# Kernel optimization log

Hardware: AMD Instinct MI355X
Metric: run time of the kernel (lower is better)

## Reference

```python
import jax, jax.numpy as jnp
import numpy as np

N_HEAD = 16
ROPE_BASE = 10000.0


def apply_rope(x):
    # x: [B, T, H, D], torchtune interleaved-pair RoPE
    B, T, H, D = x.shape
    pos = jnp.arange(T, dtype=jnp.float32)
    freqs = 1.0 / (ROPE_BASE ** (jnp.arange(0, D, 2, dtype=jnp.float32) / D))  # [D/2]
    theta = pos[:, None] * freqs[None, :]            # [T, D/2]
    cos = jnp.cos(theta)[None, :, None, :]           # [1, T, 1, D/2]
    sin = jnp.sin(theta)[None, :, None, :]
    xp = x.reshape(B, T, H, D // 2, 2)
    x0, x1 = xp[..., 0], xp[..., 1]
    out = jnp.stack([x0 * cos - x1 * sin, x1 * cos + x0 * sin], axis=-1)
    return out.reshape(B, T, H, D).astype(x.dtype)


def setup_inputs() -> dict:
    key = jax.random.key(0)
    k1, k2, k3 = jax.random.split(key, 3)
    B, T, C = 4, 2048, 1024
    x = jax.random.normal(k1, (B, T, C), dtype=jnp.float32)
    w_qkv = jax.random.normal(k2, (C, 3 * C), dtype=jnp.float32) * 0.02
    b_qkv = jnp.zeros((3 * C,), dtype=jnp.float32)
    w_proj = jax.random.normal(k3, (C, C), dtype=jnp.float32) * 0.02
    b_proj = jnp.zeros((C,), dtype=jnp.float32)
    return {"x": x, "w_qkv": w_qkv, "b_qkv": b_qkv, "w_proj": w_proj, "b_proj": b_proj}


def reference(x, w_qkv, b_qkv, w_proj, b_proj):
    B, T, C = x.shape
    H = N_HEAD
    D = C // H
    qkv = x @ w_qkv + b_qkv                          # [B, T, 3C]
    q, k, v = jnp.split(qkv, 3, axis=-1)
    q = apply_rope(q.reshape(B, T, H, D))
    k = apply_rope(k.reshape(B, T, H, D))
    v = v.reshape(B, T, H, D)
    scale = 1.0 / jnp.sqrt(jnp.asarray(D, dtype=x.dtype))
    attn = jnp.einsum('bthd,bshd->bhts', q, k) * scale  # [B, H, T, T] (non-causal)
    attn = jax.nn.softmax(attn, axis=-1)
    out = jnp.einsum('bhts,bshd->bthd', attn, v).reshape(B, T, C)
    return out @ w_proj + b_proj
```

## Files before the change

kernel.cpp:

```cpp
#include <hip/hip_runtime.h>

typedef unsigned short ushort_t;
typedef unsigned int   uint_t;
typedef __attribute__((ext_vector_type(8))) short bf16x8;
typedef __attribute__((ext_vector_type(4))) float f32x4;

__device__ __forceinline__ ushort_t f2bf(float f) {
    union { float f; uint_t i; } x; x.f = f;
    uint_t i = x.i + 0x7fffu + ((x.i >> 16) & 1u);
    return (ushort_t)(i >> 16);
}
__device__ __forceinline__ ushort_t f2bf_trunc(float f) {
    union { float f; uint_t i; } x; x.f = f;
    return (ushort_t)(x.i >> 16);
}
__device__ __forceinline__ void async16(const void* g, void* l) {
    __builtin_amdgcn_global_load_lds(
        (const __attribute__((address_space(1))) uint_t*)g,
        (__attribute__((address_space(3))) uint_t*)l, 16, 0, 0);
}

__global__ __launch_bounds__(256) void conv_bf16(
    const float* __restrict__ in, ushort_t* __restrict__ outp)
{
    int i = (blockIdx.x * 256 + threadIdx.x) * 4;
    float4 v = *(const float4*)(in + i);
    uint_t a = (uint_t)f2bf(v.x) | ((uint_t)f2bf(v.y) << 16);
    uint_t b = (uint_t)f2bf(v.z) | ((uint_t)f2bf(v.w) << 16);
    uint2 st = { a, b };
    *(uint2*)(outp + i) = st;
}

__global__ __launch_bounds__(256) void transpose_conv(
    const float* __restrict__ in, ushort_t* __restrict__ outp, int R, int C)
{
    __shared__ ushort_t t[64][65];
    int r0 = blockIdx.y * 64, c0 = blockIdx.x * 64;
    int lr = threadIdx.x >> 4, lc = (threadIdx.x & 15) * 4;
#pragma unroll
    for (int rr = 0; rr < 4; ++rr) {
        float4 v = *(const float4*)(in + (size_t)(r0 + rr * 16 + lr) * C + c0 + lc);
        t[lc + 0][rr * 16 + lr] = f2bf(v.x);
        t[lc + 1][rr * 16 + lr] = f2bf(v.y);
        t[lc + 2][rr * 16 + lr] = f2bf(v.z);
        t[lc + 3][rr * 16 + lr] = f2bf(v.w);
    }
    __syncthreads();
    int oc = threadIdx.x >> 2, och = (threadIdx.x & 3) * 16;
    union { uint4 v[2]; ushort_t u[16]; } pk;
#pragma unroll
    for (int j = 0; j < 16; ++j) pk.u[j] = t[oc][och + j];
    uint4* dst = (uint4*)(outp + (size_t)(c0 + oc) * R + r0 + och);
    dst[0] = pk.v[0]; dst[1] = pk.v[1];
}

__global__ __launch_bounds__(256) void rope_table_k(float2* __restrict__ tab)
{
    int idx = blockIdx.x * 256 + threadIdx.x;
    int t = idx >> 5, i = idx & 31;
    float freq = powf(10000.0f, -(float)i * (1.0f / 32.0f));
    float sn, cs;
    sincosf((float)t * freq, &sn, &cs);
    tab[idx] = make_float2(cs, sn);
}

template <int MODE>
__global__ __launch_bounds__(256) void gemm_mfma(
    const ushort_t* __restrict__ A, const ushort_t* __restrict__ Bt,
    const float* __restrict__ bias, void* __restrict__ Cv,
    const float2* __restrict__ tab, int M, int N, int K, int coloff)
{
    __shared__ ushort_t As[128][64];
    __shared__ ushort_t Bs[128][64];
    const int tid = threadIdx.x;
    const int w = tid >> 6, lane = tid & 63, ln = lane & 15, quad = lane >> 4;
    const int wm = w >> 1, wn = w & 1;
    const int row0 = blockIdx.y * 128, col0 = blockIdx.x * 128 + coloff;

    f32x4 acc[4][4] = {};

    const int swch = (lane & 7) ^ (lane >> 3);
    const ushort_t* ga = A  + (size_t)(row0 + w * 8 + (lane >> 3)) * K + swch * 8;
    const ushort_t* gb = Bt + (size_t)(col0 + w * 8 + (lane >> 3)) * K + swch * 8;
    ushort_t* la = &As[w * 8][0];
    ushort_t* lb = &Bs[w * 8][0];
    const int rch0 = ln & 7;

    for (int k0 = 0; k0 < K; k0 += 64) {
#pragma unroll
        for (int j = 0; j < 4; ++j) {
            async16(ga + (size_t)(j * 32) * K + k0, la + j * 32 * 64);
            async16(gb + (size_t)(j * 32) * K + k0, lb + j * 32 * 64);
        }
        __syncthreads();
#pragma unroll
        for (int kk = 0; kk < 2; ++kk) {
            int ch = ((kk * 4 + quad) ^ rch0) * 8;
            bf16x8 af[4], bfv[4];
#pragma unroll
            for (int mt = 0; mt < 4; ++mt)
                af[mt] = *(const bf16x8*)&As[wm * 64 + mt * 16 + ln][ch];
#pragma unroll
            for (int nt = 0; nt < 4; ++nt)
                bfv[nt] = *(const bf16x8*)&Bs[wn * 64 + nt * 16 + ln][ch];
#pragma unroll
            for (int mt = 0; mt < 4; ++mt)
#pragma unroll
                for (int nt = 0; nt < 4; ++nt) {
                    if (MODE == 2)
                        acc[mt][nt] = __builtin_amdgcn_mfma_f32_16x16x32_bf16(
                            af[mt], bfv[nt], acc[mt][nt], 0, 0, 0);
                    else
                        acc[mt][nt] = __builtin_amdgcn_mfma_f32_16x16x32_bf16(
                            bfv[nt], af[mt], acc[mt][nt], 0, 0, 0);
                }
        }
        __syncthreads();
    }

    if (MODE == 2) {
#pragma unroll
        for (int nt = 0; nt < 4; ++nt) {
            int c = col0 + wn * 64 + nt * 16 + ln;
            float bv = bias[c];
            int c2 = c - 2048;
            size_t vrow = ((size_t)(c2 >> 6)) * 64 + (c2 & 63);
#pragma unroll
            for (int mt = 0; mt < 4; ++mt) {
                int rr = row0 + wm * 64 + mt * 16 + quad * 4;
                int b = rr >> 11, t0 = rr & 2047;
                uint2 st;
                st.x = (uint_t)f2bf(acc[mt][nt][0] + bv)
                     | ((uint_t)f2bf(acc[mt][nt][1] + bv) << 16);
                st.y = (uint_t)f2bf(acc[mt][nt][2] + bv)
                     | ((uint_t)f2bf(acc[mt][nt][3] + bv) << 16);
                *(uint2*)((ushort_t*)Cv + ((size_t)b * 16 * 64 + vrow) * 2048 + t0) = st;
            }
        }
    } else {
#pragma unroll
        for (int mt = 0; mt < 4; ++mt) {
            int rr = row0 + wm * 64 + mt * 16 + ln;
#pragma unroll
            for (int nt = 0; nt < 4; ++nt) {
                int c0 = col0 + wn * 64 + nt * 16 + quad * 4;
                float4 bv = *(const float4*)(bias + c0);
                float v0 = acc[mt][nt][0] + bv.x, v1 = acc[mt][nt][1] + bv.y;
                float v2 = acc[mt][nt][2] + bv.z, v3 = acc[mt][nt][3] + bv.w;
                if (MODE == 1) {
                    int i0 = (c0 & 63) >> 1;
                    const float2* trow = tab + (size_t)(rr & 2047) * 32;
                    float2 cs0 = trow[i0], cs1 = trow[i0 + 1];
                    float o0 = v0 * cs0.x - v1 * cs0.y;
                    float o1 = v1 * cs0.x + v0 * cs0.y;
                    float o2 = v2 * cs1.x - v3 * cs1.y;
                    float o3 = v3 * cs1.x + v2 * cs1.y;
                    uint2 st;
                    st.x = (uint_t)f2bf(o0) | ((uint_t)f2bf(o1) << 16);
                    st.y = (uint_t)f2bf(o2) | ((uint_t)f2bf(o3) << 16);
                    *(uint2*)((ushort_t*)Cv + (size_t)rr * N + c0) = st;
                } else {
                    float4 st = { v0, v1, v2, v3 };
                    *(float4*)((float*)Cv + (size_t)rr * N + c0) = st;
                }
            }
        }
    }
}

__global__ __launch_bounds__(256, 4) void attn_mfma(
    const ushort_t* __restrict__ qkv, const ushort_t* __restrict__ vtg,
    ushort_t* __restrict__ outp)
{
    __shared__ ushort_t Ks[64][64];
    __shared__ ushort_t Vts[64][64];
    __shared__ ushort_t Ps[4][16][72];

    const int tid = threadIdx.x;
    const int w = tid >> 6, lane = tid & 63, ln = lane & 15, quad = lane >> 4;
    const int qt = blockIdx.x, bh = blockIdx.y, b = bh >> 4, h = bh & 15;
    const size_t base = (size_t)b * 2048 * 3072 + h * 64;

    bf16x8 af[2][2];
#pragma unroll
    for (int s = 0; s < 2; ++s)
#pragma unroll
        for (int kk = 0; kk < 2; ++kk)
            af[s][kk] = *(const bf16x8*)(qkv + base
                + (size_t)(qt * 128 + w * 32 + s * 16 + ln) * 3072 + kk * 32 + quad * 8);

    bf16x8 ones;
#pragma unroll
    for (int j = 0; j < 8; ++j) ones[j] = (short)0x3F80;

    f32x4 oaccT[2][4] = {};
    f32x4 oneacc[2] = {};
    const float SC = 0.125f * 1.44269504f;

    const int swch = (lane & 7) ^ (lane >> 3);
    const ushort_t* kg = qkv + base + 1024 + (size_t)(lane >> 3) * 3072 + swch * 8;
    const ushort_t* vg = vtg + ((size_t)bh * 64 + (lane >> 3)) * 2048 + swch * 8;
    const int rch0 = ln & 7;

    for (int kt = 0; kt < 32; ++kt) {
#pragma unroll
        for (int j = 0; j < 2; ++j) {
            int r8 = w * 16 + j * 8;
            async16(kg + (size_t)(kt * 64 + r8) * 3072, &Ks[r8][0]);
            async16(vg + (size_t)r8 * 2048 + kt * 64, &Vts[r8][0]);
        }
        __syncthreads();

        bf16x8 vf[2][4];
#pragma unroll
        for (int kk = 0; kk < 2; ++kk) {
            int ch = ((kk * 4 + quad) ^ rch0) * 8;
#pragma unroll
            for (int nt = 0; nt < 4; ++nt)
                vf[kk][nt] = *(const bf16x8*)&Vts[nt * 16 + ln][ch];
        }

#pragma unroll
        for (int s = 0; s < 2; ++s) {
            f32x4 sacc[4] = {};
#pragma unroll
            for (int kk = 0; kk < 2; ++kk) {
                int ch = ((kk * 4 + quad) ^ rch0) * 8;
#pragma unroll
                for (int nt = 0; nt < 4; ++nt) {
                    bf16x8 bfv = *(const bf16x8*)&Ks[nt * 16 + ln][ch];
                    sacc[nt] = __builtin_amdgcn_mfma_f32_16x16x32_bf16(
                        af[s][kk], bfv, sacc[nt], 0, 0, 0);
                }
            }

            if (s == 1)
                asm volatile("s_waitcnt lgkmcnt(0)" ::: "memory");
#pragma unroll
            for (int nt = 0; nt < 4; ++nt)
#pragma unroll
                for (int r = 0; r < 4; ++r)
                    Ps[w][quad * 4 + r][nt * 16 + ln] =
                        f2bf_trunc(exp2f(fmaf(sacc[nt][r], SC, -24.0f)));
            asm volatile("s_waitcnt lgkmcnt(0)" ::: "memory");

#pragma unroll
            for (int kk = 0; kk < 2; ++kk) {
                bf16x8 pf = *(const bf16x8*)&Ps[w][ln][kk * 32 + quad * 8];
                oneacc[s] = __builtin_amdgcn_mfma_f32_16x16x32_bf16(
                    ones, pf, oneacc[s], 0, 0, 0);
#pragma unroll
                for (int nt = 0; nt < 4; ++nt)
                    oaccT[s][nt] = __builtin_amdgcn_mfma_f32_16x16x32_bf16(
                        vf[kk][nt], pf, oaccT[s][nt], 0, 0, 0);
            }
        }
        __syncthreads();
    }

#pragma unroll
    for (int s = 0; s < 2; ++s) {
        float linv = 1.0f / oneacc[s][0];
        size_t row = (size_t)b * 2048 + qt * 128 + w * 32 + s * 16 + ln;
#pragma unroll
        for (int nt = 0; nt < 4; ++nt) {
            uint2 st;
            st.x = (uint_t)f2bf(oaccT[s][nt][0] * linv)
                 | ((uint_t)f2bf(oaccT[s][nt][1] * linv) << 16);
            st.y = (uint_t)f2bf(oaccT[s][nt][2] * linv)
                 | ((uint_t)f2bf(oaccT[s][nt][3] * linv) << 16);
            *(uint2*)(outp + row * 1024 + h * 64 + nt * 16 + quad * 4) = st;
        }
    }
}

extern "C" void kernel_launch(void* const* d_in, const int* in_sizes, int n_in,
                              void* d_out, int out_size, void* d_ws, size_t ws_size,
                              hipStream_t stream)
{
    (void)in_sizes; (void)n_in; (void)out_size; (void)ws_size;

    const float* x      = (const float*)d_in[0];
    const float* w_qkv  = (const float*)d_in[1];
    const float* b_qkv  = (const float*)d_in[2];
    const float* w_proj = (const float*)d_in[3];
    const float* b_proj = (const float*)d_in[4];
    float*       out    = (float*)d_out;

    ushort_t* x_bf    = (ushort_t*)d_ws;
    ushort_t* wqkvT   = x_bf    + (size_t)8192 * 1024;
    ushort_t* wprojT  = wqkvT   + (size_t)3072 * 1024;
    ushort_t* qkv_bf  = wprojT  + (size_t)1024 * 1024;
    ushort_t* attn_bf = qkv_bf  + (size_t)8192 * 3072;
    ushort_t* vtg     = attn_bf + (size_t)8192 * 1024;
    float2*   tab     = (float2*)(vtg + (size_t)64 * 64 * 2048);

    conv_bf16<<<8192, 256, 0, stream>>>(x, x_bf);
    transpose_conv<<<dim3(48, 16), 256, 0, stream>>>(w_qkv, wqkvT, 1024, 3072);
    transpose_conv<<<dim3(16, 16), 256, 0, stream>>>(w_proj, wprojT, 1024, 1024);
    rope_table_k<<<256, 256, 0, stream>>>(tab);

    gemm_mfma<1><<<dim3(16, 64), 256, 0, stream>>>(
        x_bf, wqkvT, b_qkv, qkv_bf, tab, 8192, 3072, 1024, 0);

    gemm_mfma<2><<<dim3(8, 64), 256, 0, stream>>>(
        x_bf, wqkvT, b_qkv, vtg, nullptr, 8192, 3072, 1024, 2048);

    attn_mfma<<<dim3(16, 64), 256, 0, stream>>>(qkv_bf, vtg, attn_bf);

    gemm_mfma<0><<<dim3(8, 64), 256, 0, stream>>>(
        attn_bf, wprojT, b_proj, out, nullptr, 8192, 1024, 1024, 0);
}
```

Before: 331.0 us.

## Double-buffer K/V tiles in attention and use 512-thread blocks

The attention kernel now double-buffers its K and V^T shared-memory tiles. The next tile's async global-to-LDS loads are issued before computing on the current one, with a single wait and barrier at the end of each iteration. Blocks grow to 8 waves covering 256 query rows, and the grid is reordered so batch-head varies fastest. This is meant to hide global load latency and halve K/V reloads per query row, at the cost of doubled LDS use and possibly lower occupancy. The prologue issues a redundant first K load into the same slot before the correct one.

Result: no change. 326.5 us (-1.4%).

```diff
diff --git a/kernel.cpp b/kernel.cpp
--- a/kernel.cpp
+++ b/kernel.cpp
@@ -168,17 +168,17 @@
     }
 }
 
-__global__ __launch_bounds__(256, 4) void attn_mfma(
+__global__ __launch_bounds__(512, 4) void attn_mfma(
     const ushort_t* __restrict__ qkv, const ushort_t* __restrict__ vtg,
     ushort_t* __restrict__ outp)
 {
-    __shared__ ushort_t Ks[64][64];
-    __shared__ ushort_t Vts[64][64];
-    __shared__ ushort_t Ps[4][16][72];
+    __shared__ ushort_t Ks[2][64][64];
+    __shared__ ushort_t Vts[2][64][64];
+    __shared__ ushort_t Ps[8][16][72];
 
     const int tid = threadIdx.x;
     const int w = tid >> 6, lane = tid & 63, ln = lane & 15, quad = lane >> 4;
-    const int qt = blockIdx.x, bh = blockIdx.y, b = bh >> 4, h = bh & 15;
+    const int bh = blockIdx.x, qt = blockIdx.y, b = bh >> 4, h = bh & 15;
     const size_t base = (size_t)b * 2048 * 3072 + h * 64;
 
     bf16x8 af[2][2];
@@ -187,7 +187,7 @@
 #pragma unroll
         for (int kk = 0; kk < 2; ++kk)
             af[s][kk] = *(const bf16x8*)(qkv + base
-                + (size_t)(qt * 128 + w * 32 + s * 16 + ln) * 3072 + kk * 32 + quad * 8);
+                + (size_t)(qt * 256 + w * 32 + s * 16 + ln) * 3072 + kk * 32 + quad * 8);
 
     bf16x8 ones;
 #pragma unroll
@@ -201,15 +201,20 @@
     const ushort_t* kg = qkv + base + 1024 + (size_t)(lane >> 3) * 3072 + swch * 8;
     const ushort_t* vg = vtg + ((size_t)bh * 64 + (lane >> 3)) * 2048 + swch * 8;
     const int rch0 = ln & 7;
-
+    const int r8 = w * 8;
+
+    async16(kg, &Ks[0][r8][0]);
+    async16(vg + (size_t)r8 * 2048, &Vts[0][r8][0]);
+    async16(kg + (size_t)r8 * 3072, &Ks[0][r8][0]);
+    asm volatile("s_waitcnt vmcnt(0)" ::: "memory");
+    __builtin_amdgcn_s_barrier();
+
+    int cur = 0;
     for (int kt = 0; kt < 32; ++kt) {
-#pragma unroll
-        for (int j = 0; j < 2; ++j) {
-            int r8 = w * 16 + j * 8;
-            async16(kg + (size_t)(kt * 64 + r8) * 3072, &Ks[r8][0]);
-            async16(vg + (size_t)r8 * 2048 + kt * 64, &Vts[r8][0]);
-        }
-        __syncthreads();
+        if (kt < 31) {
+            async16(kg + (size_t)((kt + 1) * 64 + r8) * 3072, &Ks[cur ^ 1][r8][0]);
+            async16(vg + (size_t)r8 * 2048 + (kt + 1) * 64, &Vts[cur ^ 1][r8][0]);
+        }
 
         bf16x8 vf[2][4];
 #pragma unroll
@@ -217,7 +222,7 @@
             int ch = ((kk * 4 + quad) ^ rch0) * 8;
 #pragma unroll
             for (int nt = 0; nt < 4; ++nt)
-                vf[kk][nt] = *(const bf16x8*)&Vts[nt * 16 + ln][ch];
+                vf[kk][nt] = *(const bf16x8*)&Vts[cur][nt * 16 + ln][ch];
         }
 
 #pragma unroll
@@ -228,7 +233,7 @@
                 int ch = ((kk * 4 + quad) ^ rch0) * 8;
 #pragma unroll
                 for (int nt = 0; nt < 4; ++nt) {
-                    bf16x8 bfv = *(const bf16x8*)&Ks[nt * 16 + ln][ch];
+                    bf16x8 bfv = *(const bf16x8*)&Ks[cur][nt * 16 + ln][ch];
                     sacc[nt] = __builtin_amdgcn_mfma_f32_16x16x32_bf16(
                         af[s][kk], bfv, sacc[nt], 0, 0, 0);
                 }
@@ -255,13 +260,16 @@
                         vf[kk][nt], pf, oaccT[s][nt], 0, 0, 0);
             }
         }
-        __syncthreads();
+
+        asm volatile("s_waitcnt vmcnt(0) lgkmcnt(0)" ::: "memory");
+        __builtin_amdgcn_s_barrier();
+        cur ^= 1;
     }
 
 #pragma unroll
     for (int s = 0; s < 2; ++s) {
         float linv = 1.0f / oneacc[s][0];
-        size_t row = (size_t)b * 2048 + qt * 128 + w * 32 + s * 16 + ln;
+        size_t row = (size_t)b * 2048 + qt * 256 + w * 32 + s * 16 + ln;
 #pragma unroll
         for (int nt = 0; nt < 4; ++nt) {
             uint2 st;
@@ -306,7 +314,7 @@
     gemm_mfma<2><<<dim3(8, 64), 256, 0, stream>>>(
         x_bf, wqkvT, b_qkv, vtg, nullptr, 8192, 3072, 1024, 2048);
 
-    attn_mfma<<<dim3(16, 64), 256, 0, stream>>>(qkv_bf, vtg, attn_bf);
+    attn_mfma<<<dim3(64, 8), 512, 0, stream>>>(qkv_bf, vtg, attn_bf);
 
     gemm_mfma<0><<<dim3(8, 64), 256, 0, stream>>>(
         attn_bf, wprojT, b_proj, out, nullptr, 8192, 1024, 1024, 0);
```
